# Kernel tuning notes

Hardware: AMD Instinct MI355X
Metric: run time of the kernel (lower is better)

The kernel has to match this reference:

```python
import jax, jax.numpy as jnp
import numpy as np

N0, C1, C2 = 100000, 10000, 1000
E0 = 1_600_000
IN = 128
H = 128
OUT = 128


def _pool_edges(ei, ew, cluster, C):
    # PyG pool_edge: remap via cluster, drop self loops, coalesce (sum weights)
    m = cluster[ei]
    mask = m[0] != m[1]
    m = m[:, mask]
    w = ew[mask]
    keys = m[0] * C + m[1]
    uk, inv = np.unique(keys, return_inverse=True)
    w2 = np.bincount(inv, weights=w).astype(np.float32)
    return np.stack([uk // C, uk % C]).astype(np.int64), w2


def _with_self_loops(ei, ew, N):
    # gcn_norm(add_remaining_self_loops, fill_value=1); base edges have no loops
    row = np.concatenate([ei[0], np.arange(N)]).astype(np.int64)
    col = np.concatenate([ei[1], np.arange(N)]).astype(np.int64)
    w = np.concatenate([ew, np.ones(N, np.float32)])
    return row, col, w


def setup_inputs() -> dict:
    rng = np.random.default_rng(0)
    ei = rng.integers(0, N0, size=(2, E0))
    ei = ei[:, ei[0] != ei[1]]
    ew = np.ones(ei.shape[1], np.float32)
    # guaranteed-surjective cluster assignments (stand-in for Louvain output)
    c1 = rng.permutation(np.arange(N0) % C1).astype(np.int64)
    c2 = rng.permutation(np.arange(C1) % C2).astype(np.int64)
    ei1, ew1 = _pool_edges(ei, ew, c1, C1)
    ei2, ew2 = _pool_edges(ei1, ew1, c2, C2)
    r0, co0, w0 = _with_self_loops(ei, ew, N0)
    r1, co1, w1 = _with_self_loops(ei1, ew1, C1)
    r2, co2, w2 = _with_self_loops(ei2, ew2, C2)

    key = jax.random.key(0)
    ks = jax.random.split(key, 16)
    def lin(k, fi, fo):
        return jax.random.normal(k, (fi, fo), jnp.float32) / np.sqrt(fi)
    inp = {
        'x': jax.random.normal(ks[0], (N0, IN), jnp.float32),
        'W_pre': lin(ks[1], IN, H), 'b_pre': jnp.zeros((H,), jnp.float32),
        'W_u0': lin(ks[2], H, H), 'b_u0': jnp.zeros((H,), jnp.float32),
        'W_u1': lin(ks[3], H, H), 'b_u1': jnp.zeros((H,), jnp.float32),
        'W_u2': lin(ks[4], H, H), 'b_u2': jnp.zeros((H,), jnp.float32),
        'W_d0': lin(ks[5], H, OUT), 'b_d0': jnp.zeros((OUT,), jnp.float32),
        'W_d1': lin(ks[6], H, H), 'b_d1': jnp.zeros((H,), jnp.float32),
        'row0': jnp.asarray(r0), 'col0': jnp.asarray(co0), 'ew0': jnp.asarray(w0),
        'row1': jnp.asarray(r1), 'col1': jnp.asarray(co1), 'ew1': jnp.asarray(w1),
        'row2': jnp.asarray(r2), 'col2': jnp.asarray(co2), 'ew2': jnp.asarray(w2),
        'cluster1': jnp.asarray(c1), 'cluster2': jnp.asarray(c2),
    }
    return inp


def _gcn(x, W, b, row, col, ew, N):
    # PyG GCNConv: sym-normalized aggregation at target (col)
    deg = jax.ops.segment_sum(ew, col, num_segments=N)
    dinv = jnp.where(deg > 0, jax.lax.rsqrt(deg), 0.0)
    norm = dinv[row] * ew * dinv[col]
    h = x @ W                                   # [N, F_out]
    out = jax.ops.segment_sum(h[row] * norm[:, None], col, num_segments=N)
    return out + b


def _seg_mean(x, cluster, C):
    s = jax.ops.segment_sum(x, cluster, num_segments=C)
    cnt = jax.ops.segment_sum(jnp.ones((x.shape[0], 1), x.dtype), cluster,
                              num_segments=C)
    return s / jnp.maximum(cnt, 1.0)


def reference(x, W_pre, b_pre, W_u0, b_u0, W_u1, b_u1, W_u2, b_u2,
              W_d0, b_d0, W_d1, b_d1,
              row0, col0, ew0, row1, col1, ew1, row2, col2, ew2,
              cluster1, cluster2):
    # --- up (coarsening) path ---
    h = x @ W_pre + b_pre                                   # preembed
    x0 = jax.nn.relu(_gcn(h, W_u0, b_u0, row0, col0, ew0, N0))
    x1 = _seg_mean(x0, cluster1, C1)                        # avg_pool level 1
    x1 = jax.nn.relu(_gcn(x1, W_u1, b_u1, row1, col1, ew1, C1))
    x2 = _seg_mean(x1, cluster2, C2)                        # avg_pool level 2
    x2 = jax.nn.relu(_gcn(x2, W_u2, b_u2, row2, col2, ew2, C2))
    # --- down (unpooling) path; down convs use all-ones edge weights ---
    y = x1 + x2[cluster2]
    y = jax.nn.relu(_gcn(y, W_d1, b_d1, row1, col1, jnp.ones_like(ew1), C1))
    y = x0 + y[cluster1]
    y = _gcn(y, W_d0, b_d0, row0, col0, jnp.ones_like(ew0), N0)
    return y
```

## Files before the change

### kernel.cpp

```cpp
#include <hip/hip_runtime.h>

#define HH 128
static constexpr int kN0 = 100000;
static constexpr int kC1 = 10000;
static constexpr int kC2 = 1000;

static constexpr int B0 = kN0;
static constexpr int B1 = B0 + kC1;
static constexpr int B2 = B1 + kC2;
static constexpr int B3 = B2 + kC1;
static constexpr int NTOT = B3 + kC2;

static constexpr int NB0 = (kN0 + 127) / 128;
static constexpr int NB1 = (kC1 + 7) / 8;
static constexpr int NB2 = kC2;
static constexpr int NBP1 = (kC1 + 127) / 128;
static constexpr int NBP2 = (kC2 + 15) / 16;
static constexpr int Q0 = NB0;
static constexpr int Q1 = Q0 + NB1;
static constexpr int Q2 = Q1 + NB2;
static constexpr int Q3 = Q2 + NBP1;
static constexpr int NBK = Q3 + NBP2;

__device__ __forceinline__ int bucket_of(int bin) {
  if (bin < B0) return bin >> 7;
  if (bin < B1) return Q0 + ((bin - B0) >> 3);
  if (bin < B2) return Q1 + (bin - B1);
  if (bin < B3) return Q2 + ((bin - B2) >> 7);
  return Q3 + ((bin - B3) >> 4);
}

__device__ __forceinline__ unsigned int f2_to_bf2(float a, float b) {
  unsigned int ua = __float_as_uint(a);
  unsigned int ub = __float_as_uint(b);
  ua = (ua + 0x7fffu + ((ua >> 16) & 1u)) >> 16;
  ub = (ub + 0x7fffu + ((ub >> 16) & 1u)) & 0xffff0000u;
  return ua | ub;
}

__global__ __launch_bounds__(256) void p1_kernel(const int* __restrict__ col0,
                                                 const int* __restrict__ col1,
                                                 const int* __restrict__ col2,
                                                 const int* __restrict__ cl1,
                                                 const int* __restrict__ cl2,
                                                 int E0, int E1, int E2,
                                                 int* __restrict__ bucketCnt) {
  __shared__ int h[NBK];
  for (int i = threadIdx.x; i < NBK; i += 256) h[i] = 0;
  __syncthreads();
  int T0 = E0, T1 = T0 + E1, T2 = T1 + E2, T3 = T2 + kN0, T4 = T3 + kC1;
  for (int g = blockIdx.x * 256 + threadIdx.x; g < T4; g += gridDim.x * 256) {
    int bin;
    if (g < T0)      bin = col0[g];
    else if (g < T1) bin = B0 + col1[g - T0];
    else if (g < T2) bin = B1 + col2[g - T1];
    else if (g < T3) bin = B2 + cl1[g - T2];
    else             bin = B3 + cl2[g - T3];
    atomicAdd(&h[bucket_of(bin)], 1);
  }
  __syncthreads();
  for (int i = threadIdx.x; i < NBK; i += 256) {
    int c = h[i];
    if (c) atomicAdd(&bucketCnt[i], c);
  }
}

__global__ __launch_bounds__(1024) void p2_kernel(const int* __restrict__ bucketCnt,
                                                  int* __restrict__ bucketStart,
                                                  int* __restrict__ cursor,
                                                  int* __restrict__ startsg, int T) {
  int t = threadIdx.x;
  int v[4]; int s = 0;
#pragma unroll
  for (int j = 0; j < 4; j++) {
    int i = t * 4 + j;
    v[j] = (i < NBK) ? bucketCnt[i] : 0;
    s += v[j];
  }
  int lane = t & 63, w = t >> 6;
  int incl = s;
  for (int o = 1; o < 64; o <<= 1) { int u = __shfl_up(incl, o); if (lane >= o) incl += u; }
  __shared__ int wt[16];
  if (lane == 63) wt[w] = incl;
  __syncthreads();
  if (t == 0) { int run = 0; for (int i = 0; i < 16; i++) { int c = wt[i]; wt[i] = run; run += c; } }
  __syncthreads();
  int ex = wt[w] + incl - s;
#pragma unroll
  for (int j = 0; j < 4; j++) {
    int i = t * 4 + j;
    if (i < NBK) { bucketStart[i] = ex; cursor[i] = ex; }
    ex += v[j];
  }
  if (t == 0) { bucketStart[NBK] = T; startsg[NTOT] = T; }
}

__global__ __launch_bounds__(256) void p3_kernel(const int* __restrict__ col0,
                                                 const int* __restrict__ col1,
                                                 const int* __restrict__ col2,
                                                 const int* __restrict__ cl1,
                                                 const int* __restrict__ cl2,
                                                 const int* __restrict__ row0,
                                                 const int* __restrict__ row1,
                                                 const int* __restrict__ row2,
                                                 const float* __restrict__ ew1,
                                                 const float* __restrict__ ew2,
                                                 int E0, int E1, int E2,
                                                 int* __restrict__ cursor,
                                                 int4* __restrict__ part) {
  __shared__ int h[NBK];
  __shared__ int gbase[NBK];
  for (int i = threadIdx.x; i < NBK; i += 256) h[i] = 0;
  __syncthreads();
  int T0 = E0, T1 = T0 + E1, T2 = T1 + E2, T3 = T2 + kN0, T4 = T3 + kC1;
  int base = blockIdx.x * 4096;
  int bins[16], srcs[16], rk[16];
  float wv[16];
#pragma unroll
  for (int j = 0; j < 16; j++) {
    int g = base + threadIdx.x + j * 256;
    int bin = -1, src = 0; float w = 0.f;
    if (g < T4) {
      if (g < T0) { bin = col0[g]; src = row0[g]; }
      else if (g < T1) { int e = g - T0; bin = B0 + col1[e]; src = row1[e]; w = ew1[e]; }
      else if (g < T2) { int e = g - T1; bin = B1 + col2[e]; src = row2[e]; w = ew2[e]; }
      else if (g < T3) { int e = g - T2; bin = B2 + cl1[e]; src = e; }
      else             { int e = g - T3; bin = B3 + cl2[e]; src = e; }
    }
    bins[j] = bin; srcs[j] = src; wv[j] = w;
    rk[j] = (bin >= 0) ? atomicAdd(&h[bucket_of(bin)], 1) : 0;
  }
  __syncthreads();
  for (int i = threadIdx.x; i < NBK; i += 256) {
    int c = h[i];
    gbase[i] = c ? atomicAdd(&cursor[i], c) : 0;
  }
  __syncthreads();
#pragma unroll
  for (int j = 0; j < 16; j++) {
    if (bins[j] >= 0) {
      int slot = gbase[bucket_of(bins[j])] + rk[j];
      part[slot] = make_int4(bins[j], srcs[j], __float_as_int(wv[j]), 0);
    }
  }
}

__global__ __launch_bounds__(256) void p4_kernel(const int* __restrict__ bucketStart,
                                                 const int4* __restrict__ part,
                                                 int* __restrict__ startsg,
                                                 int* __restrict__ rowS,
                                                 float* __restrict__ ewSm) {
  int b = blockIdx.x;
  int binLo, width;
  if (b < Q0)      { binLo = b << 7;                 width = 128; if (binLo + width > B0) width = B0 - binLo; }
  else if (b < Q1) { binLo = B0 + ((b - Q0) << 3);   width = 8; }
  else if (b < Q2) { binLo = B1 + (b - Q1);          width = 1; }
  else if (b < Q3) { binLo = B2 + ((b - Q2) << 7);   width = 128; if (binLo + width > B3) width = B3 - binLo; }
  else             { binLo = B3 + ((b - Q3) << 4);   width = 16; if (binLo + width > NTOT) width = NTOT - binLo; }
  int base = bucketStart[b], nend = bucketStart[b + 1];
  int t = threadIdx.x;

  if (width == 1) {
    if (t == 0) startsg[binLo] = base;
    bool isEw = (binLo >= B0 && binLo < B2);
    for (int i = base + t; i < nend; i += 256) {
      int4 it = part[i];
      rowS[i] = it.y;
      if (isEw) ewSm[i] = __int_as_float(it.z);
    }
    return;
  }

  __shared__ int h[128];
  __shared__ int cur[128];
  if (t < 128) h[t] = 0;
  __syncthreads();
  for (int i = base + t; i < nend; i += 256) atomicAdd(&h[part[i].x - binLo], 1);
  __syncthreads();
  if (t == 0) {
    int run = 0;
    for (int j = 0; j < width; j++) {
      cur[j] = run;
      startsg[binLo + j] = base + run;
      run += h[j];
    }
  }
  __syncthreads();
  for (int i = base + t; i < nend; i += 256) {
    int4 it = part[i];
    int k = it.x;
    int r = atomicAdd(&cur[k - binLo], 1);
    int dst = base + r;
    rowS[dst] = it.y;
    if (k >= B0 && k < B2) ewSm[dst] = __int_as_float(it.z);
  }
}

__global__ void dinv_kernel(const int* __restrict__ startsg, const float* __restrict__ ewSm,
                            float* __restrict__ d0, float* __restrict__ d1w,
                            float* __restrict__ d1o, float* __restrict__ d2) {
  int t = blockIdx.x * 256 + threadIdx.x;
  if (t < kN0) {
    int c = startsg[t + 1] - startsg[t];
    d0[t] = c > 0 ? rsqrtf((float)c) : 0.f;
  }
  int wid = t >> 6, lane = t & 63;
  if (wid < kC1) {
    int s = startsg[B0 + wid], e = startsg[B0 + wid + 1];
    float a = 0.f;
    for (int k = s + lane; k < e; k += 64) a += ewSm[k];
    for (int o = 32; o > 0; o >>= 1) a += __shfl_down(a, o);
    if (lane == 0) {
      d1w[wid] = a > 0.f ? rsqrtf(a) : 0.f;
      int c = e - s;
      d1o[wid] = c > 0 ? rsqrtf((float)c) : 0.f;
    }
  } else if (wid < kC1 + kC2) {
    int w2 = wid - kC1;
    int s = startsg[B1 + w2], e = startsg[B1 + w2 + 1];
    float a = 0.f;
    for (int k = s + lane; k < e; k += 64) a += ewSm[k];
    for (int o = 32; o > 0; o >>= 1) a += __shfl_down(a, o);
    if (lane == 0) d2[w2] = a > 0.f ? rsqrtf(a) : 0.f;
  }
}

__global__ void wprep_kernel(const int* __restrict__ rowS, const float* __restrict__ ewSm,
                             const float* __restrict__ dinv0, const float* __restrict__ d1w,
                             const float* __restrict__ d1o, const float* __restrict__ d2,
                             int E0, int E1, int E2,
                             float* __restrict__ wAll, float* __restrict__ w1om) {
  int e = blockIdx.x * 256 + threadIdx.x;
  int tot = E0 + E1 + E2;
  if (e >= tot) return;
  int r = rowS[e];
  if (e < E0) {
    wAll[e] = dinv0[r];
  } else if (e < E0 + E1) {
    wAll[e] = d1w[r] * ewSm[e];
    w1om[e] = d1o[r];
  } else {
    wAll[e] = d2[r] * ewSm[e];
  }
}

__global__ __launch_bounds__(256) void matmul_kernel(const float* __restrict__ X,
                                                     const float* __restrict__ Xadd,
                                                     const int* __restrict__ cl,
                                                     const float* __restrict__ W,
                                                     const float* __restrict__ bias,
                                                     float* __restrict__ Y,
                                                     unsigned int* __restrict__ Ybf, int N) {
  __shared__ float Ws[64 * 128];
  __shared__ float Xs[32 * 128];
  int t = threadIdx.x;
  int rbase = blockIdx.x * 32;
  const float4* X4 = (const float4*)X;
  float4* Xs4 = (float4*)Xs;
#pragma unroll
  for (int i = 0; i < 4; i++) {
    int idx = t + 256 * i;
    int fr = idx >> 5, fc = idx & 31;
    int row = rbase + fr; if (row >= N) row = N - 1;
    float4 v = X4[(size_t)row * 32 + fc];
    if (Xadd) {
      int c = cl[row];
      float4 u = ((const float4*)Xadd)[(size_t)c * 32 + fc];
      v.x += u.x; v.y += u.y; v.z += u.z; v.w += u.w;
    }
    Xs4[idx] = v;
  }
  float acc[4][4];
#pragma unroll
  for (int r = 0; r < 4; r++)
#pragma unroll
    for (int cc = 0; cc < 4; cc++) acc[r][cc] = 0.f;
  int c0 = (t & 31) * 4;
  int rl = (t >> 5) * 4;
  const float4* W4 = (const float4*)W;
  float4* Ws4 = (float4*)Ws;
  for (int half = 0; half < 2; half++) {
    __syncthreads();
#pragma unroll
    for (int i = 0; i < 8; i++) {
      int idx = t + 256 * i;
      Ws4[idx] = W4[half * 2048 + idx];
    }
    __syncthreads();
#pragma unroll 4
    for (int k = 0; k < 64; k++) {
      float4 w4 = *(const float4*)(Ws + k * 128 + c0);
      float xv[4];
#pragma unroll
      for (int r = 0; r < 4; r++) xv[r] = Xs[(rl + r) * 128 + half * 64 + k];
#pragma unroll
      for (int r = 0; r < 4; r++) {
        acc[r][0] = fmaf(xv[r], w4.x, acc[r][0]);
        acc[r][1] = fmaf(xv[r], w4.y, acc[r][1]);
        acc[r][2] = fmaf(xv[r], w4.z, acc[r][2]);
        acc[r][3] = fmaf(xv[r], w4.w, acc[r][3]);
      }
    }
  }
  float4 b4 = make_float4(0.f, 0.f, 0.f, 0.f);
  if (bias) b4 = *(const float4*)(bias + c0);
#pragma unroll
  for (int r = 0; r < 4; r++) {
    int row = rbase + rl + r;
    if (row < N) {
      float4 o;
      o.x = acc[r][0] + b4.x; o.y = acc[r][1] + b4.y;
      o.z = acc[r][2] + b4.z; o.w = acc[r][3] + b4.w;
      if (Ybf) {
        unsigned int pk0 = f2_to_bf2(o.x, o.y);
        unsigned int pk1 = f2_to_bf2(o.z, o.w);
        *(uint2*)(Ybf + (size_t)row * 64 + (c0 >> 1)) = make_uint2(pk0, pk1);
      } else {
        *(float4*)(Y + (size_t)row * 128 + c0) = o;
      }
    }
  }
}

__global__ __launch_bounds__(256) void agg_kernel(const unsigned int* __restrict__ Hf,
                                                  float* __restrict__ out,
                                                  const int* __restrict__ starts,
                                                  const int* __restrict__ rowS,
                                                  const float* __restrict__ wS,
                                                  const float* __restrict__ dinv,
                                                  const float* __restrict__ bias,
                                                  int C, int relu) {
  int wid = (blockIdx.x * blockDim.x + threadIdx.x) >> 6;
  int lane = threadIdx.x & 63;
  if (wid >= C) return;
  int s = starts[wid], e = starts[wid + 1];
  float dc = dinv[wid];
  float ax[4] = {0.f, 0.f, 0.f, 0.f}, ay[4] = {0.f, 0.f, 0.f, 0.f};
  for (int base = s; base < e; base += 64) {
    int n = e - base; if (n > 64) n = 64;
    int moff = base + (lane < n ? lane : 0);
    int r = rowS[moff];
    float w = wS[moff];
    int j = 0;
    for (; j + 7 < n; j += 8) {
#pragma unroll
      for (int u = 0; u < 8; u++) {
        int rr = __shfl(r, j + u);
        float ww = __shfl(w, j + u);
        unsigned int pv = Hf[(size_t)rr * 64 + lane];
        ax[u & 3] = fmaf(ww, __uint_as_float(pv << 16), ax[u & 3]);
        ay[u & 3] = fmaf(ww, __uint_as_float(pv & 0xffff0000u), ay[u & 3]);
      }
    }
    for (; j < n; j++) {
      int rr = __shfl(r, j);
      float ww = __shfl(w, j);
      unsigned int pv = Hf[(size_t)rr * 64 + lane];
      ax[0] = fmaf(ww, __uint_as_float(pv << 16), ax[0]);
      ay[0] = fmaf(ww, __uint_as_float(pv & 0xffff0000u), ay[0]);
    }
  }
  float ox = (ax[0] + ax[1] + ax[2] + ax[3]) * dc + bias[lane * 2];
  float oy = (ay[0] + ay[1] + ay[2] + ay[3]) * dc + bias[lane * 2 + 1];
  if (relu) { ox = fmaxf(ox, 0.f); oy = fmaxf(oy, 0.f); }
  *(float2*)(out + (size_t)wid * 128 + lane * 2) = make_float2(ox, oy);
}

__global__ __launch_bounds__(256) void aggb_kernel(const unsigned int* __restrict__ Hf,
                                                   float* __restrict__ out,
                                                   const int* __restrict__ starts,
                                                   const int* __restrict__ rowS,
                                                   const float* __restrict__ wS,
                                                   const float* __restrict__ dinv,
                                                   const float* __restrict__ bias,
                                                   int C, int relu) {
  int node = blockIdx.x;
  if (node >= C) return;
  int wv = threadIdx.x >> 6, lane = threadIdx.x & 63;
  int s = starts[node], e = starts[node + 1];
  float ax[4] = {0.f, 0.f, 0.f, 0.f}, ay[4] = {0.f, 0.f, 0.f, 0.f};
  for (int base = s + wv * 64; base < e; base += 256) {
    int n = e - base; if (n > 64) n = 64;
    int moff = base + (lane < n ? lane : 0);
    int r = rowS[moff];
    float w = wS[moff];
    int j = 0;
    for (; j + 7 < n; j += 8) {
#pragma unroll
      for (int u = 0; u < 8; u++) {
        int rr = __shfl(r, j + u);
        float ww = __shfl(w, j + u);
        unsigned int pv = Hf[(size_t)rr * 64 + lane];
        ax[u & 3] = fmaf(ww, __uint_as_float(pv << 16), ax[u & 3]);
        ay[u & 3] = fmaf(ww, __uint_as_float(pv & 0xffff0000u), ay[u & 3]);
      }
    }
    for (; j < n; j++) {
      int rr = __shfl(r, j);
      float ww = __shfl(w, j);
      unsigned int pv = Hf[(size_t)rr * 64 + lane];
      ax[0] = fmaf(ww, __uint_as_float(pv << 16), ax[0]);
      ay[0] = fmaf(ww, __uint_as_float(pv & 0xffff0000u), ay[0]);
    }
  }
  __shared__ float shx[256], shy[256];
  shx[threadIdx.x] = ax[0] + ax[1] + ax[2] + ax[3];
  shy[threadIdx.x] = ay[0] + ay[1] + ay[2] + ay[3];
  __syncthreads();
  if (threadIdx.x < 64) {
    float sx = shx[lane] + shx[lane + 64] + shx[lane + 128] + shx[lane + 192];
    float sy = shy[lane] + shy[lane + 64] + shy[lane + 128] + shy[lane + 192];
    float dc = dinv[node];
    float ox = sx * dc + bias[lane * 2];
    float oy = sy * dc + bias[lane * 2 + 1];
    if (relu) { ox = fmaxf(ox, 0.f); oy = fmaxf(oy, 0.f); }
    *(float2*)(out + (size_t)node * 128 + lane * 2) = make_float2(ox, oy);
  }
}

__global__ __launch_bounds__(256) void pool_kernel(const float* __restrict__ src,
                                                   float* __restrict__ out,
                                                   const int* __restrict__ starts,
                                                   const int* __restrict__ rowS, int C) {
  int wid = (blockIdx.x * blockDim.x + threadIdx.x) >> 6;
  int lane = threadIdx.x & 63;
  if (wid >= C) return;
  int s = starts[wid], e = starts[wid + 1];
  float ax0 = 0.f, ay0 = 0.f, ax1 = 0.f, ay1 = 0.f;
  int m = s;
  for (; m + 3 < e; m += 4) {
    int i0 = rowS[m], i1 = rowS[m + 1], i2 = rowS[m + 2], i3 = rowS[m + 3];
    float2 v0 = *(const float2*)(src + (size_t)i0 * 128 + lane * 2);
    float2 v1 = *(const float2*)(src + (size_t)i1 * 128 + lane * 2);
    float2 v2 = *(const float2*)(src + (size_t)i2 * 128 + lane * 2);
    float2 v3 = *(const float2*)(src + (size_t)i3 * 128 + lane * 2);
    ax0 += v0.x; ay0 += v0.y;
    ax1 += v1.x; ay1 += v1.y;
    ax0 += v2.x; ay0 += v2.y;
    ax1 += v3.x; ay1 += v3.y;
  }
  for (; m < e; m++) {
    int id = rowS[m];
    const float2 v = *(const float2*)(src + (size_t)id * 128 + lane * 2);
    ax0 += v.x; ay0 += v.y;
  }
  float inv = (e > s) ? 1.f / (float)(e - s) : 0.f;
  *(float2*)(out + (size_t)wid * 128 + lane * 2) =
      make_float2((ax0 + ax1) * inv, (ay0 + ay1) * inv);
}

__global__ void addgather_kernel(const float* __restrict__ a, const float* __restrict__ b,
                                 const int* __restrict__ cl, float* __restrict__ out, int nrows) {
  int g = blockIdx.x * 256 + threadIdx.x;
  if (g >= nrows * 32) return;
  int rowi = g >> 5;
  int c = cl[rowi];
  float4 va = ((const float4*)a)[g];
  float4 vb = ((const float4*)b)[(size_t)c * 32 + (g & 31)];
  float4 o;
  o.x = va.x + vb.x; o.y = va.y + vb.y; o.z = va.z + vb.z; o.w = va.w + vb.w;
  ((float4*)out)[g] = o;
}


extern "C" void kernel_launch(void* const* d_in, const int* in_sizes, int n_in,
                              void* d_out, int out_size, void* d_ws, size_t ws_size,
                              hipStream_t stream) {
  const float* x     = (const float*)d_in[0];
  const float* W_pre = (const float*)d_in[1];
  const float* b_pre = (const float*)d_in[2];
  const float* W_u0  = (const float*)d_in[3];
  const float* b_u0  = (const float*)d_in[4];
  const float* W_u1  = (const float*)d_in[5];
  const float* b_u1  = (const float*)d_in[6];
  const float* W_u2  = (const float*)d_in[7];
  const float* b_u2  = (const float*)d_in[8];
  const float* W_d0  = (const float*)d_in[9];
  const float* b_d0  = (const float*)d_in[10];
  const float* W_d1  = (const float*)d_in[11];
  const float* b_d1  = (const float*)d_in[12];
  const int* row0 = (const int*)d_in[13];
  const int* col0 = (const int*)d_in[14];
  const int* row1 = (const int*)d_in[16];
  const int* col1 = (const int*)d_in[17];
  const float* ew1 = (const float*)d_in[18];
  const int* row2 = (const int*)d_in[19];
  const int* col2 = (const int*)d_in[20];
  const float* ew2 = (const float*)d_in[21];
  const int* cluster1 = (const int*)d_in[22];
  const int* cluster2 = (const int*)d_in[23];
  int E0 = in_sizes[13], E1 = in_sizes[16], E2 = in_sizes[19];
  float* out = (float*)d_out;
  int Ttot = E0 + E1 + E2 + kN0 + kC1;
  int Etot = E0 + E1 + E2;

  char* basep = (char*)d_ws;
  size_t off = 0;
  auto alloc = [&](size_t bytes) -> char* {
    char* p = basep + off;
    off = (off + bytes + 255) & ~(size_t)255;
    return p;
  };
  int* bucketCnt = (int*)alloc((size_t)NBK * 4);
  size_t zero_bytes = off;
  int* bucketStart = (int*)alloc((size_t)(NBK + 1) * 4);
  int* cursor      = (int*)alloc((size_t)NBK * 4);
  int* startsg     = (int*)alloc((size_t)(NTOT + 1) * 4);
  int* rowS  = (int*)alloc((size_t)Ttot * 4);
  float* ewS = (float*)alloc((size_t)(E1 + E2) * 4);
  float* ewSm = ewS - E0;
  float* dinv0  = (float*)alloc((size_t)kN0 * 4);
  float* dinv1w = (float*)alloc((size_t)kC1 * 4);
  float* dinv1o = (float*)alloc((size_t)kC1 * 4);
  float* dinv2  = (float*)alloc((size_t)kC2 * 4);
  size_t watermark = off;
  int4* part = (int4*)alloc((size_t)Ttot * 16);
  off = watermark;
  float* wAll = (float*)alloc((size_t)Etot * 4);
  float* w1o  = (float*)alloc((size_t)E1 * 4);
  float* w1om = w1o - E0;
  float* A    = (float*)alloc((size_t)kN0 * HH * 4);
  float* s1a  = (float*)alloc((size_t)kC1 * HH * 4);
  float* s1b  = (float*)alloc((size_t)kC1 * HH * 4);
  float* s2a  = (float*)alloc((size_t)kC2 * HH * 4);
  unsigned int* s1bb = (unsigned int*)alloc((size_t)kC1 * 64 * 4);
  unsigned int* s2bb = (unsigned int*)alloc((size_t)kC2 * 64 * 4);
  unsigned int* s1cb = (unsigned int*)alloc((size_t)kC1 * 64 * 4);
  unsigned int* tb   = (unsigned int*)alloc((size_t)kN0 * 64 * 4);
  unsigned int* t0   = (unsigned int*)d_out;

  hipMemsetAsync(d_ws, 0, zero_bytes, stream);

  auto cdiv = [](int a, int b) { return (a + b - 1) / b; };

  p1_kernel<<<256, 256, 0, stream>>>(col0, col1, col2, cluster1, cluster2, E0, E1, E2, bucketCnt);
  p2_kernel<<<1, 1024, 0, stream>>>(bucketCnt, bucketStart, cursor, startsg, Ttot);
  p3_kernel<<<cdiv(Ttot, 4096), 256, 0, stream>>>(col0, col1, col2, cluster1, cluster2,
                                                  row0, row1, row2, ew1, ew2, E0, E1, E2,
                                                  cursor, part);
  p4_kernel<<<NBK, 256, 0, stream>>>(bucketStart, part, startsg, rowS, ewSm);
  dinv_kernel<<<cdiv((kC1 + kC2) * 64, 256), 256, 0, stream>>>(startsg, ewSm, dinv0, dinv1w,
                                                               dinv1o, dinv2);
  wprep_kernel<<<cdiv(Etot, 256), 256, 0, stream>>>(rowS, ewSm, dinv0, dinv1w, dinv1o, dinv2,
                                                    E0, E1, E2, wAll, w1om);

  matmul_kernel<<<cdiv(kN0, 32), 256, 0, stream>>>(x, nullptr, nullptr, W_pre, b_pre, A, nullptr, kN0);
  matmul_kernel<<<cdiv(kN0, 32), 256, 0, stream>>>(A, nullptr, nullptr, W_u0, nullptr, nullptr, t0, kN0);
  agg_kernel<<<cdiv(kN0, 4), 256, 0, stream>>>(t0, A, startsg, rowS, wAll, dinv0, b_u0, kN0, 1);
  pool_kernel<<<cdiv(kC1, 4), 256, 0, stream>>>(A, s1a, startsg + B2, rowS, kC1);
  matmul_kernel<<<cdiv(kC1, 32), 256, 0, stream>>>(s1a, nullptr, nullptr, W_u1, nullptr, nullptr, s1bb, kC1);
  aggb_kernel<<<kC1, 256, 0, stream>>>(s1bb, s1a, startsg + B0, rowS, wAll, dinv1w, b_u1, kC1, 1);
  pool_kernel<<<cdiv(kC2, 4), 256, 0, stream>>>(s1a, s2a, startsg + B3, rowS, kC2);
  matmul_kernel<<<cdiv(kC2, 32), 256, 0, stream>>>(s2a, nullptr, nullptr, W_u2, nullptr, nullptr, s2bb, kC2);
  aggb_kernel<<<kC2, 256, 0, stream>>>(s2bb, s2a, startsg + B1, rowS, wAll, dinv2, b_u2, kC2, 1);
  matmul_kernel<<<cdiv(kC1, 32), 256, 0, stream>>>(s1a, s2a, cluster2, W_d1, nullptr, nullptr, s1cb, kC1);
  aggb_kernel<<<kC1, 256, 0, stream>>>(s1cb, s1b, startsg + B0, rowS, w1om, dinv1o, b_d1, kC1, 1);
  addgather_kernel<<<cdiv(kN0 * 32, 256), 256, 0, stream>>>(A, s1b, cluster1, A, kN0);
  matmul_kernel<<<cdiv(kN0, 32), 256, 0, stream>>>(A, nullptr, nullptr, W_d0, nullptr, nullptr, tb, kN0);
  agg_kernel<<<cdiv(kN0, 4), 256, 0, stream>>>(tb, out, startsg, rowS, wAll, dinv0, b_d0, kN0, 0);
}
```

Measured before the change: 774.6 us.

## Fold preembed into conv weights, chunk bf16 features, and fuse unpool gather

Precomputes W_pre·W_u0 and b_pre·W_u0 so the first GCN needs one large matmul instead of two. The big-graph bf16 features are stored in 8 feature-chunks of 16 columns, and aggregation runs per chunk with 8 edges in flight per wavefront, aiming to keep the gathered working set cache-resident. The level-0 edge weights are computed on the fly from dinv, which removes the level-0 part of wprep. The unpool add-gather is fused into the final matmul's load. The trade-off is more aggregation blocks, a cross-lane reduction, and some rounding differences from the weight folding.

```diff
diff --git a/kernel.cpp b/kernel.cpp
--- a/kernel.cpp
+++ b/kernel.cpp
@@ -21,6 +21,8 @@
 static constexpr int Q2 = Q1 + NB2;
 static constexpr int Q3 = Q2 + NBP1;
 static constexpr int NBK = Q3 + NBP2;
+
+static constexpr int NCHUNK = 8;
 
 __device__ __forceinline__ int bucket_of(int bin) {
   if (bin < B0) return bin >> 7;
@@ -226,17 +228,15 @@
 }
 
 __global__ void wprep_kernel(const int* __restrict__ rowS, const float* __restrict__ ewSm,
-                             const float* __restrict__ dinv0, const float* __restrict__ d1w,
+                             const float* __restrict__ d1w,
                              const float* __restrict__ d1o, const float* __restrict__ d2,
                              int E0, int E1, int E2,
                              float* __restrict__ wAll, float* __restrict__ w1om) {
-  int e = blockIdx.x * 256 + threadIdx.x;
+  int e = blockIdx.x * 256 + threadIdx.x + E0;
   int tot = E0 + E1 + E2;
   if (e >= tot) return;
   int r = rowS[e];
-  if (e < E0) {
-    wAll[e] = dinv0[r];
-  } else if (e < E0 + E1) {
+  if (e < E0 + E1) {
     wAll[e] = d1w[r] * ewSm[e];
     w1om[e] = d1o[r];
   } else {
@@ -250,7 +250,8 @@
                                                      const float* __restrict__ W,
                                                      const float* __restrict__ bias,
                                                      float* __restrict__ Y,
-                                                     unsigned int* __restrict__ Ybf, int N) {
+                                                     unsigned int* __restrict__ Ybf,
+                                                     int bfChunkN, int N) {
   __shared__ float Ws[64 * 128];
   __shared__ float Xs[32 * 128];
   int t = threadIdx.x;
@@ -314,7 +315,13 @@
       if (Ybf) {
         unsigned int pk0 = f2_to_bf2(o.x, o.y);
         unsigned int pk1 = f2_to_bf2(o.z, o.w);
-        *(uint2*)(Ybf + (size_t)row * 64 + (c0 >> 1)) = make_uint2(pk0, pk1);
+        int p0 = c0 >> 1;
+        if (bfChunkN) {
+          size_t addr = ((size_t)(p0 >> 3) * bfChunkN + row) * 8 + (p0 & 7);
+          *(uint2*)(Ybf + addr) = make_uint2(pk0, pk1);
+        } else {
+          *(uint2*)(Ybf + (size_t)row * 64 + p0) = make_uint2(pk0, pk1);
+        }
       } else {
         *(float4*)(Y + (size_t)row * 128 + c0) = o;
       }
@@ -322,48 +329,51 @@
   }
 }
 
-__global__ __launch_bounds__(256) void agg_kernel(const unsigned int* __restrict__ Hf,
-                                                  float* __restrict__ out,
-                                                  const int* __restrict__ starts,
-                                                  const int* __restrict__ rowS,
-                                                  const float* __restrict__ wS,
-                                                  const float* __restrict__ dinv,
-                                                  const float* __restrict__ bias,
-                                                  int C, int relu) {
-  int wid = (blockIdx.x * blockDim.x + threadIdx.x) >> 6;
+__global__ __launch_bounds__(256) void aggc_kernel(const unsigned int* __restrict__ Hfc,
+                                                   float* __restrict__ out,
+                                                   const int* __restrict__ starts,
+                                                   const int* __restrict__ rowS,
+                                                   const float* __restrict__ dinv,
+                                                   const float* __restrict__ bias,
+                                                   int C, int relu) {
+  int nblk = (C + 3) >> 2;
+  int chunk = blockIdx.x / nblk;
+  int wid = (blockIdx.x - chunk * nblk) * 4 + (threadIdx.x >> 6);
+  if (wid >= C) return;
   int lane = threadIdx.x & 63;
-  if (wid >= C) return;
+  int f = lane & 7, g = lane >> 3;
   int s = starts[wid], e = starts[wid + 1];
-  float dc = dinv[wid];
-  float ax[4] = {0.f, 0.f, 0.f, 0.f}, ay[4] = {0.f, 0.f, 0.f, 0.f};
+  const unsigned int* Tf = Hfc + (size_t)chunk * C * 8 + f;
+  float ax = 0.f, ay = 0.f;
   for (int base = s; base < e; base += 64) {
     int n = e - base; if (n > 64) n = 64;
     int moff = base + (lane < n ? lane : 0);
     int r = rowS[moff];
-    float w = wS[moff];
-    int j = 0;
-    for (; j + 7 < n; j += 8) {
-#pragma unroll
-      for (int u = 0; u < 8; u++) {
-        int rr = __shfl(r, j + u);
-        float ww = __shfl(w, j + u);
-        unsigned int pv = Hf[(size_t)rr * 64 + lane];
-        ax[u & 3] = fmaf(ww, __uint_as_float(pv << 16), ax[u & 3]);
-        ay[u & 3] = fmaf(ww, __uint_as_float(pv & 0xffff0000u), ay[u & 3]);
+    float w = (lane < n) ? dinv[r] : 0.f;
+    for (int j = 0; j < n; j += 32) {
+#pragma unroll
+      for (int u = 0; u < 4; u++) {
+        int src = j + u * 8 + g;
+        if (src > 63) src = 63;
+        int rr = __shfl(r, src);
+        float ww = __shfl(w, src);
+        unsigned int pv = Tf[(size_t)rr * 8];
+        ax = fmaf(ww, __uint_as_float(pv << 16), ax);
+        ay = fmaf(ww, __uint_as_float(pv & 0xffff0000u), ay);
       }
     }
-    for (; j < n; j++) {
-      int rr = __shfl(r, j);
-      float ww = __shfl(w, j);
-      unsigned int pv = Hf[(size_t)rr * 64 + lane];
-      ax[0] = fmaf(ww, __uint_as_float(pv << 16), ax[0]);
-      ay[0] = fmaf(ww, __uint_as_float(pv & 0xffff0000u), ay[0]);
-    }
-  }
-  float ox = (ax[0] + ax[1] + ax[2] + ax[3]) * dc + bias[lane * 2];
-  float oy = (ay[0] + ay[1] + ay[2] + ay[3]) * dc + bias[lane * 2 + 1];
-  if (relu) { ox = fmaxf(ox, 0.f); oy = fmaxf(oy, 0.f); }
-  *(float2*)(out + (size_t)wid * 128 + lane * 2) = make_float2(ox, oy);
+  }
+  ax += __shfl_xor(ax, 8);  ay += __shfl_xor(ay, 8);
+  ax += __shfl_xor(ax, 16); ay += __shfl_xor(ay, 16);
+  ax += __shfl_xor(ax, 32); ay += __shfl_xor(ay, 32);
+  if (g == 0) {
+    float dc = dinv[wid];
+    int fo = chunk * 16 + f * 2;
+    float ox = ax * dc + bias[fo];
+    float oy = ay * dc + bias[fo + 1];
+    if (relu) { ox = fmaxf(ox, 0.f); oy = fmaxf(oy, 0.f); }
+    *(float2*)(out + (size_t)wid * 128 + fo) = make_float2(ox, oy);
+  }
 }
 
 __global__ __launch_bounds__(256) void aggb_kernel(const unsigned int* __restrict__ Hf,
@@ -447,19 +457,6 @@
   float inv = (e > s) ? 1.f / (float)(e - s) : 0.f;
   *(float2*)(out + (size_t)wid * 128 + lane * 2) =
       make_float2((ax0 + ax1) * inv, (ay0 + ay1) * inv);
-}
-
-__global__ void addgather_kernel(const float* __restrict__ a, const float* __restrict__ b,
-                                 const int* __restrict__ cl, float* __restrict__ out, int nrows) {
-  int g = blockIdx.x * 256 + threadIdx.x;
-  if (g >= nrows * 32) return;
-  int rowi = g >> 5;
-  int c = cl[rowi];
-  float4 va = ((const float4*)a)[g];
-  float4 vb = ((const float4*)b)[(size_t)c * 32 + (g & 31)];
-  float4 o;
-  o.x = va.x + vb.x; o.y = va.y + vb.y; o.z = va.z + vb.z; o.w = va.w + vb.w;
-  ((float4*)out)[g] = o;
 }
 
 
@@ -519,6 +516,8 @@
   float* wAll = (float*)alloc((size_t)Etot * 4);
   float* w1o  = (float*)alloc((size_t)E1 * 4);
   float* w1om = w1o - E0;
+  float* Wf   = (float*)alloc((size_t)128 * 128 * 4);
+  float* bfv  = (float*)alloc((size_t)128 * 4);
   float* A    = (float*)alloc((size_t)kN0 * HH * 4);
   float* s1a  = (float*)alloc((size_t)kC1 * HH * 4);
   float* s1b  = (float*)alloc((size_t)kC1 * HH * 4);
@@ -541,21 +540,28 @@
   p4_kernel<<<NBK, 256, 0, stream>>>(bucketStart, part, startsg, rowS, ewSm);
   dinv_kernel<<<cdiv((kC1 + kC2) * 64, 256), 256, 0, stream>>>(startsg, ewSm, dinv0, dinv1w,
                                                                dinv1o, dinv2);
-  wprep_kernel<<<cdiv(Etot, 256), 256, 0, stream>>>(rowS, ewSm, dinv0, dinv1w, dinv1o, dinv2,
-                                                    E0, E1, E2, wAll, w1om);
-
-  matmul_kernel<<<cdiv(kN0, 32), 256, 0, stream>>>(x, nullptr, nullptr, W_pre, b_pre, A, nullptr, kN0);
-  matmul_kernel<<<cdiv(kN0, 32), 256, 0, stream>>>(A, nullptr, nullptr, W_u0, nullptr, nullptr, t0, kN0);
-  agg_kernel<<<cdiv(kN0, 4), 256, 0, stream>>>(t0, A, startsg, rowS, wAll, dinv0, b_u0, kN0, 1);
+  wprep_kernel<<<cdiv(E1 + E2, 256), 256, 0, stream>>>(rowS, ewSm, dinv1w, dinv1o, dinv2,
+                                                       E0, E1, E2, wAll, w1om);
+
+  matmul_kernel<<<cdiv(128, 32), 256, 0, stream>>>(W_pre, nullptr, nullptr, W_u0, nullptr,
+                                                   Wf, nullptr, 0, 128);
+  matmul_kernel<<<1, 256, 0, stream>>>(b_pre, nullptr, nullptr, W_u0, nullptr,
+                                       bfv, nullptr, 0, 1);
+  matmul_kernel<<<cdiv(kN0, 32), 256, 0, stream>>>(x, nullptr, nullptr, Wf, bfv,
+                                                   nullptr, t0, kN0, kN0);
+  aggc_kernel<<<NCHUNK * cdiv(kN0, 4), 256, 0, stream>>>(t0, A, startsg, rowS, dinv0, b_u0, kN0, 1);
   pool_kernel<<<cdiv(kC1, 4), 256, 0, stream>>>(A, s1a, startsg + B2, rowS, kC1);
-  matmul_kernel<<<cdiv(kC1, 32), 256, 0, stream>>>(s1a, nullptr, nullptr, W_u1, nullptr, nullptr, s1bb, kC1);
+  matmul_kernel<<<cdiv(kC1, 32), 256, 0, stream>>>(s1a, nullptr, nullptr, W_u1, nullptr,
+                                                   nullptr, s1bb, 0, kC1);
   aggb_kernel<<<kC1, 256, 0, stream>>>(s1bb, s1a, startsg + B0, rowS, wAll, dinv1w, b_u1, kC1, 1);
   pool_kernel<<<cdiv(kC2, 4), 256, 0, stream>>>(s1a, s2a, startsg + B3, rowS, kC2);
-  matmul_kernel<<<cdiv(kC2, 32), 256, 0, stream>>>(s2a, nullptr, nullptr, W_u2, nullptr, nullptr, s2bb, kC2);
+  matmul_kernel<<<cdiv(kC2, 32), 256, 0, stream>>>(s2a, nullptr, nullptr, W_u2, nullptr,
+                                                   nullptr, s2bb, 0, kC2);
   aggb_kernel<<<kC2, 256, 0, stream>>>(s2bb, s2a, startsg + B1, rowS, wAll, dinv2, b_u2, kC2, 1);
-  matmul_kernel<<<cdiv(kC1, 32), 256, 0, stream>>>(s1a, s2a, cluster2, W_d1, nullptr, nullptr, s1cb, kC1);
+  matmul_kernel<<<cdiv(kC1, 32), 256, 0, stream>>>(s1a, s2a, cluster2, W_d1, nullptr,
+                                                   nullptr, s1cb, 0, kC1);
   aggb_kernel<<<kC1, 256, 0, stream>>>(s1cb, s1b, startsg + B0, rowS, w1om, dinv1o, b_d1, kC1, 1);
-  addgather_kernel<<<cdiv(kN0 * 32, 256), 256, 0, stream>>>(A, s1b, cluster1, A, kN0);
-  matmul_kernel<<<cdiv(kN0, 32), 256, 0, stream>>>(A, nullptr, nullptr, W_d0, nullptr, nullptr, tb, kN0);
-  agg_kernel<<<cdiv(kN0, 4), 256, 0, stream>>>(tb, out, startsg, rowS, wAll, dinv0, b_d0, kN0, 0);
-}
+  matmul_kernel<<<cdiv(kN0, 32), 256, 0, stream>>>(A, s1b, cluster1, W_d0, nullptr,
+                                                   nullptr, tb, kN0, kN0);
+  aggc_kernel<<<NCHUNK * cdiv(kN0, 4), 256, 0, stream>>>(tb, out, startsg, rowS, dinv0, b_d0, kN0, 0);
+}
```

After: 1.023 ms. 32.0% more time.
